# Kernel tuning notes

Hardware: AMD Instinct MI355X
Metric: run time of the kernel (lower is better)

The kernel has to match this reference:

```python
import jax, jax.numpy as jnp
import numpy as np

N, E = 32768, 262144
IN_C, OUT_C = 128, 128
N_GRAPHS = 64


def setup_inputs() -> dict:
    key = jax.random.key(0)
    ks = jax.random.split(key, 8)
    x = jax.random.normal(ks[0], (N, IN_C), dtype=jnp.float32)
    edge_index = jax.random.randint(ks[1], (2, E), 0, N, dtype=jnp.int32)
    batch = jnp.sort(jax.random.randint(ks[2], (N,), 0, N_GRAPHS, dtype=jnp.int32))
    rand = jax.random.uniform(ks[3], (E,), dtype=jnp.float32)  # replaces random.random() draws
    lim_t = 1.0 / np.sqrt(IN_C)
    W_t = jax.random.uniform(ks[4], (IN_C, OUT_C), jnp.float32, -lim_t, lim_t)
    b_t = jax.random.uniform(ks[5], (OUT_C,), jnp.float32, -lim_t, lim_t)
    lim_s = 1.0 / np.sqrt(OUT_C)
    W_s = jax.random.uniform(ks[6], (OUT_C, 1), jnp.float32, -lim_s, lim_s)
    b_s = jax.random.uniform(ks[7], (1,), jnp.float32, -lim_s, lim_s)
    return dict(x=x, edge_index=edge_index, batch=batch, rand=rand,
                W_t=W_t, b_t=b_t, W_s=W_s, b_s=b_s)


def _greedy_match(scores, src, dst, rand, n):
    """Sequential greedy edge matching over score-sorted edges.
    Returns (order, cid_sorted, n_merged): cid_sorted[i] is the cluster id
    assigned to sorted edge i, or -1 if rejected/skipped."""
    scores = jax.lax.stop_gradient(scores)  # indices are non-differentiable (torch uses .item())
    rand = jax.lax.stop_gradient(rand)
    order = jnp.argsort(-scores)
    s_o, d_o = src[order], dst[order]
    acc = rand[order] <= scores[order]  # torch: skip edge if r > edge_score

    def step(carry, inp):
        avail, nxt = carry
        s, t, a = inp
        ok = a & avail[s] & avail[t]
        cid = jnp.where(ok, nxt, -1)
        avail = avail.at[s].set(avail[s] & ~ok)
        avail = avail.at[t].set(avail[t] & ~ok)
        return (avail, nxt + ok.astype(jnp.int32)), cid

    (_, n_merged), cid_sorted = jax.lax.scan(
        step, (jnp.ones((n,), bool), jnp.int32(0)), (s_o, d_o, acc))
    return order, cid_sorted, n_merged


def reference(x, edge_index, batch, rand, W_t, b_t, W_s, b_s):
    n = x.shape[0]
    src, dst = edge_index[0], edge_index[1]
    # merge_edge_sum + transform (eval mode, dropout p=0)
    x_merged = (x[src] + x[dst]) @ W_t + b_t          # [E, OUT_C]
    x_self = (x + x) @ W_t + b_t                      # [N, OUT_C] (self-edge merge)
    e = jax.nn.sigmoid((x_merged @ W_s).reshape(-1) + b_s[0])  # [E] edge scores

    order, cid_sorted, n_merged = _greedy_match(e, src, dst, rand, n)
    ok = cid_sorted >= 0                              # accepted sorted edges
    s_o, d_o = src[order], dst[order]

    # node -> cluster assignment (sentinel index n is dropped)
    cluster = jnp.full((n,), -1, jnp.int32)
    cluster = cluster.at[jnp.where(ok, s_o, n)].set(cid_sorted, mode='drop')
    cluster = cluster.at[jnp.where(ok, d_o, n)].set(cid_sorted, mode='drop')
    remaining = cluster < 0
    rem_rank = jnp.cumsum(remaining.astype(jnp.int32)) - 1  # ascending node order, like set iteration
    cluster = jnp.where(remaining, n_merged + rem_rank, cluster)
    num_clusters = n_merged + remaining.sum().astype(jnp.int32)

    # pooled features, padded to [n, OUT_C]; rows [0, num_clusters) are valid
    mcid = jnp.where(ok, cid_sorted, n)
    new_x = jnp.zeros((n, x_merged.shape[1]), x.dtype)
    new_x = new_x.at[mcid].set(x_merged[order], mode='drop')
    new_x = new_x.at[jnp.where(remaining, cluster, n)].set(x_self, mode='drop')

    # per-cluster edge score (1.0 for unmerged singleton nodes)
    new_edge_score = jnp.ones((n,), e.dtype).at[mcid].set(e[order], mode='drop')

    # new batch vector: new_batch[cluster[v]] = batch[v]
    new_batch = jnp.zeros((n,), batch.dtype).at[cluster].set(batch)

    # remapped edges + coalesce/remove_self_loops expressed as a validity mask
    new_ei = cluster[edge_index]                      # [2, E]
    key = new_ei[0].astype(jnp.int64) * n + new_ei[1].astype(jnp.int64)
    perm = jnp.argsort(key)
    ksorted = key[perm]
    first = jnp.concatenate([jnp.array([True]), ksorted[1:] != ksorted[:-1]])
    unique = jnp.zeros((key.shape[0],), bool).at[perm].set(first)
    edge_valid = unique & (new_ei[0] != new_ei[1])

    return new_x, cluster, new_batch, new_edge_score, num_clusters, new_ei, edge_valid, e
```

## Files before the change

kernel.cpp:

```cpp
#include <hip/hip_runtime.h>
#include <stdint.h>

typedef unsigned int u32;
typedef unsigned long long u64;

#define NN 32768
#define NE 262144
#define NC 128

#define O0 0u
#define O1 4194304u
#define O2 4227072u
#define O3 4259840u
#define O4 4292608u
#define O5 4292609u
#define O6 4816897u
#define O7 5079041u

#define HCAP (1u<<19)
#define NFULL 8
#define CNT0 8
#define MCAP 16384
#define SCAP 32768
#define SNB 32
#define MAXK 0xFFFFFFFFFFFFFFFFull
#define EMASK 0x3FFFFu

__global__ void ep_init(const float* Wt, const float* Ws, const float* bt, const float* bs,
                        double* u, double* c0, u32* counters,
                        u64* b0, u64* b1, u32* avail, int* cl,
                        u32* tkey, u32* tmin, unsigned char* premat) {
    u32 i = blockIdx.x*blockDim.x + threadIdx.x;
    if (blockIdx.x == 0 && threadIdx.x < 128) {
        int r = threadIdx.x;
        double s = 0.0;
        for (int j = 0; j < NC; j++) s += (double)Wt[r*NC+j] * (double)Ws[j];
        u[r] = s;
        if (r == 0) {
            double c = 0.0;
            for (int j = 0; j < NC; j++) c += (double)bt[j] * (double)Ws[j];
            *c0 = c + (double)bs[0];
        }
    }
    if (i < 64) counters[i] = 0u;
    if (i < NN) { b0[i] = MAXK; b1[i] = MAXK; cl[i] = -1; }
    if (i < NN/32) avail[i] = 0xFFFFFFFFu;
    ((unsigned short*)premat)[i] = 0;
    for (u32 j = i; j < HCAP; j += 131072u) { tkey[j] = 0xFFFFFFFFu; tmin[j] = 0xFFFFFFFFu; }
}

__global__ void ep_ynode(const float* x, const double* u, double* y) {
    int gid = blockIdx.x*blockDim.x + threadIdx.x;
    int v = gid >> 6, lane = threadIdx.x & 63;
    if (v >= NN) return;
    double t = (double)x[v*NC+lane]*u[lane] + (double)x[v*NC+lane+64]*u[lane+64];
    for (int off = 32; off; off >>= 1) t += __shfl_down(t, off, 64);
    if (lane == 0) y[v] = t;
}

__global__ void ep_escore(const int* src, const int* dst, const float* rnd, const double* y,
                          const double* c0, u64* fkey, u32* counters, float* out) {
    int e = blockIdx.x*blockDim.x + threadIdx.x;
    if (e >= NE) return;
    int s = src[e], d = dst[e];
    double z = y[s] + y[d] + *c0;
    double sc = 1.0/(1.0 + exp(-z));
    out[O7 + e] = (float)sc;
    u64 b = (u64)__double_as_longlong(z);
    u64 ord = (b & 0x8000000000000000ull) ? ~b : (b | 0x8000000000000000ull);
    u64 P = ((~ord) & 0xFFFFFFFFFFFC0000ull) | (u64)(u32)e;
    if ((double)rnd[e] <= sc) {
        u32 p = atomicAdd(&counters[CNT0], 1u);
        fkey[p] = P;
    }
}

__device__ __forceinline__ bool ep_bit(const u32* a, u32 v) { return (a[v>>5] >> (v&31)) & 1u; }

__global__ void ep_rA(const u64* fkey, const int* src, const int* dst,
                      const u32* cnt, u64* bt, const u32* avail) {
    u32 n = *cnt;
    for (u32 i = blockIdx.x*blockDim.x + threadIdx.x; i < n; i += 65536u) {
        u64 P = fkey[i];
        u32 e = (u32)(P & EMASK);
        u32 s = (u32)src[e], d = (u32)dst[e];
        if (ep_bit(avail, s) && ep_bit(avail, d)) {
            atomicMin(&bt[s], P); atomicMin(&bt[d], P);
        }
    }
}

__global__ void ep_rB(const u64* fkey, const int* src, const int* dst,
                      const u32* cnt, u32* cntN, u64* fkeyN,
                      const u64* bt, u64* btN, u32* avail,
                      u64* mkey, unsigned char* premat, u32* counters) {
    u32 n = *cnt;
    for (u32 i = blockIdx.x*blockDim.x + threadIdx.x; i < n; i += 65536u) {
        u64 P = fkey[i];
        u32 e = (u32)(P & EMASK);
        u32 s = (u32)src[e], d = (u32)dst[e];
        if (!ep_bit(avail, s) || !ep_bit(avail, d)) continue;
        if (bt[s] == P && bt[d] == P) {
            u32 slot = atomicAdd(&counters[2], 1u);
            mkey[slot] = P;
            premat[e] = 1;
            atomicAnd(&avail[s>>5], ~(1u<<(s&31)));
            atomicAnd(&avail[d>>5], ~(1u<<(d&31)));
        } else {
            u32 p = atomicAdd(cntN, 1u);
            fkeyN[p] = P;
            btN[s] = MAXK; btN[d] = MAXK;
        }
    }
}

__global__ void ep_merge(const u64* mk, const u64* fk, u32* counters, u64* ck) {
    u32 i = blockIdx.x*blockDim.x + threadIdx.x;
    u32 nm0 = counters[2];
    u32 cr  = counters[CNT0+NFULL];
    if (i == 0) { u32 tot = nm0 + cr; counters[4] = tot > SCAP ? SCAP : tot; }
    u64 K = MAXK;
    if (i < nm0) K = mk[i];
    else if (i < nm0 + cr && i < SCAP) K = fk[i-nm0];
    ck[i] = K;
}

__device__ __forceinline__ u64 ep_peers(u32 d, bool real) {
    u64 m = ~0ull;
    #pragma unroll
    for (int b = 0; b < 8; b++) {
        u64 bb = __ballot((d >> b) & 1u);
        m &= ((d >> b) & 1u) ? bb : ~bb;
    }
    return m & __ballot(real);
}

__global__ void ms_hist(const u64* key, u32* hist, int shift, const u32* counters) {
    __shared__ u32 h[256];
    int t = threadIdx.x;
    u32 total = counters[4];
    h[t] = 0; h[t+64] = 0; h[t+128] = 0; h[t+192] = 0;
    u32 blk = blockIdx.x;
    for (int j = 0; j < 16; j++) {
        u32 idx = blk*1024u + (u32)j*64u + (u32)t;
        bool real = idx < total;
        u64 k = real ? key[idx] : MAXK;
        u32 d = (u32)(k >> shift) & 255u;
        u64 m = ep_peers(d, real);
        if (real && t == (__ffsll((unsigned long long)m) - 1)) h[d] += (u32)__popcll(m);
    }
    hist[(u32)t*SNB + blk]       = h[t];
    hist[((u32)t+64)*SNB + blk]  = h[t+64];
    hist[((u32)t+128)*SNB + blk] = h[t+128];
    hist[((u32)t+192)*SNB + blk] = h[t+192];
}

__global__ void ms_scan(u32* hist) {
    __shared__ u32 w[4];
    int t = threadIdx.x;
    int base = t*32;
    u32 s = 0;
    for (int j = 0; j < 32; j++) s += hist[base+j];
    u32 x = s;
    for (int off = 1; off < 64; off <<= 1) { u32 yv = __shfl_up(x, off, 64); if ((t&63) >= off) x += yv; }
    if ((t&63) == 63) w[t>>6] = x;
    __syncthreads();
    if (t == 0) { u32 a = 0; for (int k = 0; k < 4; k++) { u32 tmp = w[k]; w[k] = a; a += tmp; } }
    __syncthreads();
    u32 run = w[t>>6] + x - s;
    for (int j = 0; j < 32; j++) { u32 tmp = hist[base+j]; hist[base+j] = run; run += tmp; }
}

__global__ void ms_scat(const u64* ki, u64* ko, const u32* hist, int shift, const u32* counters) {
    __shared__ u32 cnt[256];
    int t = threadIdx.x;
    u32 total = counters[4];
    cnt[t] = 0; cnt[t+64] = 0; cnt[t+128] = 0; cnt[t+192] = 0;
    u32 blk = blockIdx.x;
    for (int j = 0; j < 16; j++) {
        u32 idx = blk*1024u + (u32)j*64u + (u32)t;
        bool real = idx < total;
        u64 k = real ? ki[idx] : MAXK;
        u32 d = (u32)(k >> shift) & 255u;
        u64 m = ep_peers(d, real);
        if (real) {
            u32 rank = (u32)__popcll(m & (((u64)1 << t) - 1ull));
            int leader = __ffsll((unsigned long long)m) - 1;
            u32 base = 0;
            if (t == leader) { base = cnt[d]; cnt[d] = base + (u32)__popcll(m); }
            base = __shfl(base, leader, 64);
            ko[hist[d*SNB + blk] + base + rank] = k;
        }
    }
}

__global__ void ep_csum(const u64* sk, const unsigned char* premat, const u32* counters,
                        u32* mflag, u32* csums) {
    u32 i = blockIdx.x*1024 + threadIdx.x;
    u32 cnt = counters[4];
    bool pre = (i < cnt) && premat[(u32)(sk[i] & EMASK)];
    bool cand = (i < cnt) && !pre;
    mflag[i] = pre ? 1u : 0u;
    int c = __syncthreads_count(cand ? 1 : 0);
    if (threadIdx.x == 0) csums[blockIdx.x] = (u32)c;
}

__global__ void ep_cscan(u32* csums, u32* counters, int which) {
    int t = threadIdx.x;
    u32 v = (t < SNB) ? csums[t] : 0u;
    u32 x = v;
    for (int off = 1; off < 64; off <<= 1) { u32 y = __shfl_up(x, off, 64); if (t >= off) x += y; }
    if (t < SNB) csums[t] = x - v;
    if (t == SNB-1) counters[which] = x;
}

__global__ void ep_cemit(const u64* sk, const unsigned char* premat, const u32* counters,
                         const u32* csums, u32* candIdx) {
    __shared__ u32 w[16];
    int t = threadIdx.x;
    u32 i = blockIdx.x*1024 + t;
    u32 cnt = counters[4];
    bool pre = (i < cnt) && premat[(u32)(sk[i] & EMASK)];
    u32 c = ((i < cnt) && !pre) ? 1u : 0u;
    u32 x = c;
    for (int off = 1; off < 64; off <<= 1) { u32 y = __shfl_up(x, off, 64); if ((t&63) >= off) x += y; }
    if ((t&63) == 63) w[t>>6] = x;
    __syncthreads();
    if (t < 16) {
        u32 ww = w[t];
        for (int off = 1; off < 16; off <<= 1) { u32 y = __shfl_up(ww, off, 16); if (t >= off) ww += y; }
        w[t] = ww;
    }
    __syncthreads();
    u32 excl = ((t>>6) ? w[(t>>6)-1] : 0u) + x - c;
    if (c) candIdx[csums[blockIdx.x] + excl] = i;
}

__global__ void __launch_bounds__(512) ep_walk(const u64* sk, const int* src, const int* dst,
                                               const u32* candIdx, u32* counters,
                                               const u32* availG, u32* mflag, u32* msums) {
    __shared__ u32 avail[1024];
    __shared__ u32 claim[16384];
    __shared__ u32 part[512];
    __shared__ u32 segs[32];
    int t = threadIdx.x;
    avail[t] = availG[t]; avail[t+512] = availG[t+512];
    for (int j = t; j < 16384; j += 512) claim[j] = 0xFFFFFFFFu;
    __syncthreads();
    u32 ncand = counters[5];
    u32 iterTag = 0x3FFFFFu;
    for (u32 base = 0; base < ncand; base += 512) {
        u32 j = base + (u32)t;
        bool have = j < ncand;
        u32 i = 0, s = 0, d = 0;
        if (have) {
            i = candIdx[j];
            u32 e = (u32)(sk[i] & EMASK);
            s = (u32)src[e]; d = (u32)dst[e];
        }
        u32 hs = s & 16383u, hd = d & 16383u;
        int st = 1;
        if (have && ((avail[s>>5]>>(s&31))&1u) && ((avail[d>>5]>>(d&31))&1u)) st = 0;
        for (int guard = 0; guard < 4096; guard++) {
            u32 tag = (iterTag << 10) | (u32)t;
            if (st == 0) { atomicMin(&claim[hs], tag); atomicMin(&claim[hd], tag); }
            __syncthreads();
            if (st == 0) {
                bool aok = ((avail[s>>5]>>(s&31))&1u) && ((avail[d>>5]>>(d&31))&1u);
                if (!aok) st = 1;
                else if (claim[hs] == tag && claim[hd] == tag) {
                    st = 2;
                    atomicAnd(&avail[s>>5], ~(1u<<(s&31)));
                    atomicAnd(&avail[d>>5], ~(1u<<(d&31)));
                    mflag[i] = 1u;
                }
            }
            iterTag--;
            if (__syncthreads_count(st == 0) == 0) break;
        }
    }
    __syncthreads();
    u32 p = 0; int b2 = t*64;
    for (int j = 0; j < 64; j++) p += mflag[b2+j];
    part[t] = p;
    __syncthreads();
    if (t < 32) { u32 sg = 0; for (int j = 0; j < 16; j++) sg += part[t*16+j]; segs[t] = sg; }
    __syncthreads();
    if (t == 0) { u32 a = 0; for (int g = 0; g < 32; g++) { msums[g] = a; a += segs[g]; } counters[2] = a; }
}

__global__ void ep_memit(const u64* sk, const int* src, const int* dst,
                         const u32* mflag, const u32* msums,
                         const int* batch, u64* Mlist, int* cl, float* out) {
    __shared__ u32 w[16];
    int t = threadIdx.x;
    u32 i = blockIdx.x*1024 + t;
    u32 m = mflag[i];
    u32 x = m;
    for (int off = 1; off < 64; off <<= 1) { u32 y = __shfl_up(x, off, 64); if ((t&63) >= off) x += y; }
    if ((t&63) == 63) w[t>>6] = x;
    __syncthreads();
    if (t < 16) {
        u32 ww = w[t];
        for (int off = 1; off < 16; off <<= 1) { u32 y = __shfl_up(ww, off, 16); if (t >= off) ww += y; }
        w[t] = ww;
    }
    __syncthreads();
    u32 excl = ((t>>6) ? w[(t>>6)-1] : 0u) + x - m;
    if (m) {
        u32 cid = msums[blockIdx.x] + excl;
        u32 e = (u32)(sk[i] & EMASK);
        u32 s = (u32)src[e], d = (u32)dst[e];
        Mlist[cid] = ((u64)e << 30) | ((u64)s << 15) | (u64)d;
        cl[s] = (int)cid; cl[d] = (int)cid;
        u32 mx = s > d ? s : d;
        out[O2 + cid] = (float)batch[mx];
        out[O3 + cid] = out[O7 + e];
    }
}

__global__ void ep_scanN(int* cl, u32* counters, u32* slist, float* out) {
    __shared__ u32 w[16];
    int t = threadIdx.x;
    int base = t*32;
    u32 s = 0;
    for (int j = 0; j < 32; j++) s += (cl[base+j] < 0) ? 1u : 0u;
    u32 x = s;
    for (int off = 1; off < 64; off <<= 1) { u32 y = __shfl_up(x, off, 64); if ((t&63) >= off) x += y; }
    if ((t&63) == 63) w[t>>6] = x;
    __syncthreads();
    if (t < 16) {
        u32 ww = w[t];
        for (int off = 1; off < 16; off <<= 1) { u32 y = __shfl_up(ww, off, 16); if (t >= off) ww += y; }
        w[t] = ww;
    }
    __syncthreads();
    u32 excl = ((t>>6) ? w[(t>>6)-1] : 0u) + x - s;
    u32 total = w[15];
    u32 nm = counters[2];
    if (t == 0) {
        counters[3] = nm + total;
        counters[6] = total;
        out[O4] = (float)(nm + total);
    }
    u32 run = nm + excl;
    for (int j = 0; j < 32; j++) {
        if (cl[base+j] < 0) {
            slist[run - nm] = (u32)(base + j);
            cl[base+j] = (int)(run++);
        }
    }
}

__global__ void ep_out_nodes(const int* cl, const int* batch, const u32* counters, float* out) {
    int v = blockIdx.x*blockDim.x + threadIdx.x;
    if (v >= NN) return;
    u32 nm = counters[2], ncl = counters[3];
    int c = cl[v];
    out[O1 + v] = (float)c;
    if (c >= (int)nm) out[O2 + c] = (float)batch[v];
    if (v >= (int)nm) out[O3 + v] = 1.0f;
    if (v >= (int)ncl) out[O2 + v] = 0.0f;
}

__global__ void ep_newx_m(const float* x, const float* Wt, const float* bt,
                          const u64* Mlist, const u32* counters, float* out) {
    __shared__ u64 ml[32];
    __shared__ float m[32][128];
    u32 nm = counters[2];
    u32 base = blockIdx.x * 32u;
    if (base >= nm) return;
    int t = threadIdx.x, lane = t & 63, wv = t >> 6;
    if (t < 32) { u32 r = base + (u32)t; ml[t] = (r < nm) ? Mlist[r] : 0ull; }
    __syncthreads();
    for (int i = t; i < 4096; i += 256) {
        int r = i >> 7, k = i & 127;
        u64 v = ml[r];
        u32 s = (u32)((v>>15)&0x7FFF), d = (u32)(v&0x7FFF);
        m[r][k] = x[s*NC+k] + x[d*NC+k];
    }
    __syncthreads();
    float a0[8], a1[8];
    #pragma unroll
    for (int r = 0; r < 8; r++) { a0[r] = bt[lane]; a1[r] = bt[lane+64]; }
    for (int k = 0; k < 128; k++) {
        float w0 = Wt[k*NC+lane], w1 = Wt[k*NC+lane+64];
        #pragma unroll
        for (int r = 0; r < 8; r++) { float mm = m[wv*8+r][k]; a0[r] += mm*w0; a1[r] += mm*w1; }
    }
    #pragma unroll
    for (int r = 0; r < 8; r++) {
        u32 row = base + (u32)(wv*8 + r);
        if (row < nm) {
            out[O0 + (size_t)row*NC + lane]      = a0[r];
            out[O0 + (size_t)row*NC + lane + 64] = a1[r];
        }
    }
}

__global__ void ep_newx_s(const float* x, const float* Wt, const float* bt,
                          const u32* slist, const u32* counters, float* out) {
    __shared__ u32 nodes[32];
    __shared__ float m[32][128];
    u32 nm = counters[2], ncl = counters[3], sc = counters[6];
    u32 base = nm + blockIdx.x * 32u;
    if (base >= NN) return;
    int t = threadIdx.x, lane = t & 63, wv = t >> 6;
    if (base >= ncl) {
        for (int i = t; i < 4096; i += 256) {
            u32 row = base + (u32)(i >> 7);
            if (row < NN) out[O0 + (size_t)row*NC + (i & 127)] = 0.0f;
        }
        return;
    }
    if (t < 32) { u32 p = base - nm + (u32)t; nodes[t] = (p < sc) ? slist[p] : slist[0]; }
    __syncthreads();
    for (int i = t; i < 4096; i += 256) {
        int r = i >> 7, k = i & 127;
        m[r][k] = 2.0f * x[nodes[r]*NC + k];
    }
    __syncthreads();
    float a0[8], a1[8];
    #pragma unroll
    for (int r = 0; r < 8; r++) { a0[r] = bt[lane]; a1[r] = bt[lane+64]; }
    for (int k = 0; k < 128; k++) {
        float w0 = Wt[k*NC+lane], w1 = Wt[k*NC+lane+64];
        #pragma unroll
        for (int r = 0; r < 8; r++) { float mm = m[wv*8+r][k]; a0[r] += mm*w0; a1[r] += mm*w1; }
    }
    #pragma unroll
    for (int r = 0; r < 8; r++) {
        u32 row = base + (u32)(wv*8 + r);
        if (row >= NN) continue;
        if (row < ncl) {
            out[O0 + (size_t)row*NC + lane]      = a0[r];
            out[O0 + (size_t)row*NC + lane + 64] = a1[r];
        } else {
            out[O0 + (size_t)row*NC + lane]      = 0.0f;
            out[O0 + (size_t)row*NC + lane + 64] = 0.0f;
        }
    }
}

__global__ void ep_newei(const int* src, const int* dst, const int* cl,
                         u32* tkey, u32* tmin, u32* eslot, float* out) {
    int e = blockIdx.x*blockDim.x + threadIdx.x;
    if (e >= NE) return;
    u32 cs = (u32)cl[src[e]], cd = (u32)cl[dst[e]];
    out[O5 + e]      = (float)cs;
    out[O5 + NE + e] = (float)cd;
    u32 key = (cs << 15) | cd;
    u32 slot = ((key * 2654435761u) >> 11) & (HCAP-1);
    while (true) {
        u32 k = tkey[slot];
        if (k == key) break;
        if (k == 0xFFFFFFFFu) {
            u32 old = atomicCAS(&tkey[slot], 0xFFFFFFFFu, key);
            if (old == 0xFFFFFFFFu || old == key) break;
        }
        slot = (slot + 1) & (HCAP-1);
    }
    eslot[e] = slot | ((cs != cd) ? 0x80000000u : 0u);
    atomicMin(&tmin[slot], (u32)e);
}

__global__ void ep_valid(const u32* tmin, const u32* eslot, float* out) {
    int e = blockIdx.x*blockDim.x + threadIdx.x;
    if (e >= NE) return;
    u32 sl = eslot[e];
    bool valid = (tmin[sl & 0x7FFFFFFFu] == (u32)e) && (sl >> 31);
    out[O6 + e] = valid ? 1.0f : 0.0f;
}

extern "C" void kernel_launch(void* const* d_in, const int* in_sizes, int n_in,
                              void* d_out, int out_size, void* d_ws, size_t ws_size,
                              hipStream_t stream) {
    (void)in_sizes; (void)n_in; (void)out_size; (void)ws_size;
    const float* x    = (const float*)d_in[0];
    const int*   ei   = (const int*)d_in[1];
    const int*   src  = ei;
    const int*   dst  = ei + NE;
    const int*   batch= (const int*)d_in[2];
    const float* rnd  = (const float*)d_in[3];
    const float* Wt   = (const float*)d_in[4];
    const float* bt   = (const float*)d_in[5];
    const float* Ws   = (const float*)d_in[6];
    const float* bs   = (const float*)d_in[7];
    float* out = (float*)d_out;

    char* w = (char*)d_ws;
    double* u  = (double*)w;
    double* c0 = (double*)(w + 1024);
    u32* counters = (u32*)(w + 2048);
    size_t off = 4096;
    double* y   = (double*)(w + off); off += (size_t)NN*8;
    u64* fkeyA  = (u64*)(w + off); off += (size_t)NE*8;
    u64* fkeyB  = (u64*)(w + off); off += (size_t)NE*8;
    u64* mkeyA  = (u64*)(w + off); off += (size_t)MCAP*8;
    u64* combK  = (u64*)(w + off); off += (size_t)SCAP*8;
    u64* combK2 = (u64*)(w + off); off += (size_t)SCAP*8;
    u64* bt0    = (u64*)(w + off); off += (size_t)NN*8;
    u64* bt1    = (u64*)(w + off); off += (size_t)NN*8;
    u32* avail  = (u32*)(w + off); off += NN/8;
    int* cl     = (int*)(w + off); off += (size_t)NN*4;
    u64* Mlist  = (u64*)(w + off); off += (size_t)NN*8;
    u32* hist   = (u32*)(w + off); off += 8192*4;
    u32* mflag  = (u32*)(w + off); off += (size_t)SCAP*4;
    u32* candIdx= (u32*)(w + off); off += (size_t)SCAP*4;
    u32* csums  = (u32*)(w + off); off += 64*4;
    u32* msums  = (u32*)(w + off); off += 64*4;
    u32* slist  = (u32*)(w + off); off += (size_t)NN*4;
    unsigned char* premat = (unsigned char*)(w + off); off += NE;
    u32* tkey   = (u32*)(w + off); off += (size_t)HCAP*4;
    u32* tmin   = (u32*)(w + off); off += (size_t)HCAP*4;
    u32* eslot  = (u32*)(w + off); off += (size_t)NE*4;

    ep_init<<<512, 256, 0, stream>>>(Wt, Ws, bt, bs, u, c0, counters,
                                     bt0, bt1, avail, cl, tkey, tmin, premat);
    ep_ynode<<<8192, 256, 0, stream>>>(x, u, y);
    ep_escore<<<1024, 256, 0, stream>>>(src, dst, rnd, y, c0, fkeyA, counters, out);

    u64 *fk = fkeyA, *fk2 = fkeyB;
    u64 *bc = bt0, *bn = bt1;
    for (u32 rd = 0; rd < NFULL; rd++) {
        ep_rA<<<256, 256, 0, stream>>>(fk, src, dst, &counters[CNT0+rd], bc, avail);
        ep_rB<<<256, 256, 0, stream>>>(fk, src, dst, &counters[CNT0+rd], &counters[CNT0+rd+1],
                                       fk2, bc, bn, avail, mkeyA, premat, counters);
        u64* tp;
        tp = fk; fk = fk2; fk2 = tp;
        tp = bc; bc = bn; bn = tp;
    }

    ep_merge<<<SNB, 1024, 0, stream>>>(mkeyA, fk, counters, combK);
    u64 *ki = combK, *ko = combK2;
    for (int p = 0; p < 6; p++) {
        int shift = 16 + p*8;
        ms_hist<<<SNB, 64, 0, stream>>>(ki, hist, shift, counters);
        ms_scan<<<1, 256, 0, stream>>>(hist);
        ms_scat<<<SNB, 64, 0, stream>>>(ki, ko, hist, shift, counters);
        u64* tp = ki; ki = ko; ko = tp;
    }

    ep_csum<<<SNB, 1024, 0, stream>>>(combK, premat, counters, mflag, csums);
    ep_cscan<<<1, 64, 0, stream>>>(csums, counters, 5);
    ep_cemit<<<SNB, 1024, 0, stream>>>(combK, premat, counters, csums, candIdx);
    ep_walk<<<1, 512, 0, stream>>>(combK, src, dst, candIdx, counters, avail, mflag, msums);
    ep_memit<<<SNB, 1024, 0, stream>>>(combK, src, dst, mflag, msums, batch, Mlist, cl, out);

    ep_scanN<<<1, 1024, 0, stream>>>(cl, counters, slist, out);
    ep_out_nodes<<<128, 256, 0, stream>>>(cl, batch, counters, out);

    ep_newx_m<<<512, 256, 0, stream>>>(x, Wt, bt, Mlist, counters, out);
    ep_newx_s<<<1024, 256, 0, stream>>>(x, Wt, bt, slist, counters, out);

    ep_newei<<<1024, 256, 0, stream>>>(src, dst, cl, tkey, tmin, eslot, out);
    ep_valid<<<1024, 256, 0, stream>>>(tmin, eslot, out);
}
```

Before: 717.4 us.

## Fuse radix sort passes into one persistent kernel and merge walk stages

The six-pass radix sort, previously three launches per pass, becomes a single persistent 32-block kernel that separates hist, scan and scatter with a software grid barrier built on global atomics. The candidate compaction, greedy walk, merged-list emission and singleton scan, previously six separate kernels, are folded into one 1024-thread single-block kernel. The aim is to cut roughly two dozen small kernel launches and their serialization gaps. In exchange it relies on all 32 blocks being co-resident for the spin barrier, and it moves the emit and scan work onto a single block.

```diff
diff --git a/kernel.cpp b/kernel.cpp
--- a/kernel.cpp
+++ b/kernel.cpp
@@ -135,121 +135,123 @@
     return m & __ballot(real);
 }
 
-__global__ void ms_hist(const u64* key, u32* hist, int shift, const u32* counters) {
+__device__ __forceinline__ void ms_gbar(u32* bar) {
+    __syncthreads();
+    if (threadIdx.x == 0) {
+        __threadfence();
+        u32 gen = atomicAdd(&bar[1], 0u);
+        if (atomicAdd(&bar[0], 1u) == SNB - 1) {
+            atomicExch(&bar[0], 0u);
+            __threadfence();
+            atomicAdd(&bar[1], 1u);
+        } else {
+            while (atomicAdd(&bar[1], 0u) == gen) __builtin_amdgcn_s_sleep(8);
+        }
+        __threadfence();
+    }
+    __syncthreads();
+}
+
+__global__ void __launch_bounds__(64) ms_sort(u64* a, u64* b, u32* hist,
+                                              const u32* counters, u32* bar) {
     __shared__ u32 h[256];
     int t = threadIdx.x;
+    u32 blk = blockIdx.x;
     u32 total = counters[4];
-    h[t] = 0; h[t+64] = 0; h[t+128] = 0; h[t+192] = 0;
-    u32 blk = blockIdx.x;
-    for (int j = 0; j < 16; j++) {
-        u32 idx = blk*1024u + (u32)j*64u + (u32)t;
-        bool real = idx < total;
-        u64 k = real ? key[idx] : MAXK;
-        u32 d = (u32)(k >> shift) & 255u;
-        u64 m = ep_peers(d, real);
-        if (real && t == (__ffsll((unsigned long long)m) - 1)) h[d] += (u32)__popcll(m);
-    }
-    hist[(u32)t*SNB + blk]       = h[t];
-    hist[((u32)t+64)*SNB + blk]  = h[t+64];
-    hist[((u32)t+128)*SNB + blk] = h[t+128];
-    hist[((u32)t+192)*SNB + blk] = h[t+192];
-}
-
-__global__ void ms_scan(u32* hist) {
-    __shared__ u32 w[4];
-    int t = threadIdx.x;
-    int base = t*32;
-    u32 s = 0;
-    for (int j = 0; j < 32; j++) s += hist[base+j];
-    u32 x = s;
-    for (int off = 1; off < 64; off <<= 1) { u32 yv = __shfl_up(x, off, 64); if ((t&63) >= off) x += yv; }
-    if ((t&63) == 63) w[t>>6] = x;
-    __syncthreads();
-    if (t == 0) { u32 a = 0; for (int k = 0; k < 4; k++) { u32 tmp = w[k]; w[k] = a; a += tmp; } }
-    __syncthreads();
-    u32 run = w[t>>6] + x - s;
-    for (int j = 0; j < 32; j++) { u32 tmp = hist[base+j]; hist[base+j] = run; run += tmp; }
-}
-
-__global__ void ms_scat(const u64* ki, u64* ko, const u32* hist, int shift, const u32* counters) {
-    __shared__ u32 cnt[256];
-    int t = threadIdx.x;
-    u32 total = counters[4];
-    cnt[t] = 0; cnt[t+64] = 0; cnt[t+128] = 0; cnt[t+192] = 0;
-    u32 blk = blockIdx.x;
-    for (int j = 0; j < 16; j++) {
-        u32 idx = blk*1024u + (u32)j*64u + (u32)t;
-        bool real = idx < total;
-        u64 k = real ? ki[idx] : MAXK;
-        u32 d = (u32)(k >> shift) & 255u;
-        u64 m = ep_peers(d, real);
-        if (real) {
-            u32 rank = (u32)__popcll(m & (((u64)1 << t) - 1ull));
-            int leader = __ffsll((unsigned long long)m) - 1;
-            u32 base = 0;
-            if (t == leader) { base = cnt[d]; cnt[d] = base + (u32)__popcll(m); }
-            base = __shfl(base, leader, 64);
-            ko[hist[d*SNB + blk] + base + rank] = k;
-        }
-    }
-}
-
-__global__ void ep_csum(const u64* sk, const unsigned char* premat, const u32* counters,
-                        u32* mflag, u32* csums) {
-    u32 i = blockIdx.x*1024 + threadIdx.x;
-    u32 cnt = counters[4];
-    bool pre = (i < cnt) && premat[(u32)(sk[i] & EMASK)];
-    bool cand = (i < cnt) && !pre;
-    mflag[i] = pre ? 1u : 0u;
-    int c = __syncthreads_count(cand ? 1 : 0);
-    if (threadIdx.x == 0) csums[blockIdx.x] = (u32)c;
-}
-
-__global__ void ep_cscan(u32* csums, u32* counters, int which) {
-    int t = threadIdx.x;
-    u32 v = (t < SNB) ? csums[t] : 0u;
-    u32 x = v;
-    for (int off = 1; off < 64; off <<= 1) { u32 y = __shfl_up(x, off, 64); if (t >= off) x += y; }
-    if (t < SNB) csums[t] = x - v;
-    if (t == SNB-1) counters[which] = x;
-}
-
-__global__ void ep_cemit(const u64* sk, const unsigned char* premat, const u32* counters,
-                         const u32* csums, u32* candIdx) {
-    __shared__ u32 w[16];
-    int t = threadIdx.x;
-    u32 i = blockIdx.x*1024 + t;
-    u32 cnt = counters[4];
-    bool pre = (i < cnt) && premat[(u32)(sk[i] & EMASK)];
-    u32 c = ((i < cnt) && !pre) ? 1u : 0u;
-    u32 x = c;
-    for (int off = 1; off < 64; off <<= 1) { u32 y = __shfl_up(x, off, 64); if ((t&63) >= off) x += y; }
-    if ((t&63) == 63) w[t>>6] = x;
-    __syncthreads();
-    if (t < 16) {
-        u32 ww = w[t];
-        for (int off = 1; off < 16; off <<= 1) { u32 y = __shfl_up(ww, off, 16); if (t >= off) ww += y; }
-        w[t] = ww;
-    }
-    __syncthreads();
-    u32 excl = ((t>>6) ? w[(t>>6)-1] : 0u) + x - c;
-    if (c) candIdx[csums[blockIdx.x] + excl] = i;
-}
-
-__global__ void __launch_bounds__(512) ep_walk(const u64* sk, const int* src, const int* dst,
-                                               const u32* candIdx, u32* counters,
-                                               const u32* availG, u32* mflag, u32* msums) {
+    u64 *ki = a, *ko = b;
+    for (int p = 0; p < 6; p++) {
+        int shift = 16 + p*8;
+        h[t] = 0; h[t+64] = 0; h[t+128] = 0; h[t+192] = 0;
+        for (int j = 0; j < 16; j++) {
+            u32 idx = blk*1024u + (u32)j*64u + (u32)t;
+            bool real = idx < total;
+            u64 k = real ? ki[idx] : MAXK;
+            u32 d = (u32)(k >> shift) & 255u;
+            u64 m = ep_peers(d, real);
+            if (real && t == (__ffsll((unsigned long long)m) - 1)) h[d] += (u32)__popcll(m);
+        }
+        hist[(u32)t*SNB + blk]       = h[t];
+        hist[((u32)t+64)*SNB + blk]  = h[t+64];
+        hist[((u32)t+128)*SNB + blk] = h[t+128];
+        hist[((u32)t+192)*SNB + blk] = h[t+192];
+        ms_gbar(bar);
+        if (blk == 0) {
+            int b2 = t*128;
+            u32 s = 0;
+            for (int j = 0; j < 128; j++) s += hist[b2+j];
+            u32 x = s;
+            for (int off = 1; off < 64; off <<= 1) { u32 yv = __shfl_up(x, off, 64); if (t >= off) x += yv; }
+            u32 run = x - s;
+            for (int j = 0; j < 128; j++) { u32 tmp = hist[b2+j]; hist[b2+j] = run; run += tmp; }
+        }
+        ms_gbar(bar);
+        h[t] = 0; h[t+64] = 0; h[t+128] = 0; h[t+192] = 0;
+        for (int j = 0; j < 16; j++) {
+            u32 idx = blk*1024u + (u32)j*64u + (u32)t;
+            bool real = idx < total;
+            u64 k = real ? ki[idx] : MAXK;
+            u32 d = (u32)(k >> shift) & 255u;
+            u64 m = ep_peers(d, real);
+            if (real) {
+                u32 rank = (u32)__popcll(m & (((u64)1 << t) - 1ull));
+                int leader = __ffsll((unsigned long long)m) - 1;
+                u32 base = 0;
+                if (t == leader) { base = h[d]; h[d] = base + (u32)__popcll(m); }
+                base = __shfl(base, leader, 64);
+                ko[hist[d*SNB + blk] + base + rank] = k;
+            }
+        }
+        ms_gbar(bar);
+        u64* tp = ki; ki = ko; ko = tp;
+    }
+}
+
+__global__ void __launch_bounds__(1024) ep_walk(const u64* sk, const int* src, const int* dst,
+                                                const unsigned char* premat, u32* counters,
+                                                const u32* availG, u32* mflag, u32* candIdx,
+                                                u64* Mlist, int* cl, u32* slist,
+                                                const int* batch, float* out) {
     __shared__ u32 avail[1024];
     __shared__ u32 claim[16384];
-    __shared__ u32 part[512];
-    __shared__ u32 segs[32];
+    __shared__ u32 wsc[16];
     int t = threadIdx.x;
-    avail[t] = availG[t]; avail[t+512] = availG[t+512];
-    for (int j = t; j < 16384; j += 512) claim[j] = 0xFFFFFFFFu;
-    __syncthreads();
-    u32 ncand = counters[5];
+    avail[t] = availG[t];
+    for (int j = t; j < 16384; j += 1024) claim[j] = 0xFFFFFFFFu;
+    u32 total = counters[4];
+    int b32 = t*32;
+
+    u32 premask = 0, havemask = 0, cc = 0;
+    for (int j = 0; j < 32; j++) {
+        u32 i = (u32)(b32 + j);
+        u32 have = (i < total) ? 1u : 0u;
+        u32 pre = 0;
+        if (have) pre = premat[(u32)(sk[i] & EMASK)] ? 1u : 0u;
+        mflag[i] = pre;
+        premask |= pre << j;
+        havemask |= have << j;
+        cc += have & ~pre & 1u;
+    }
+    __syncthreads();
+    u32 x = cc;
+    for (int off = 1; off < 64; off <<= 1) { u32 y = __shfl_up(x, off, 64); if ((t&63) >= off) x += y; }
+    if ((t&63) == 63) wsc[t>>6] = x;
+    __syncthreads();
+    if (t < 16) {
+        u32 ww = wsc[t];
+        for (int off = 1; off < 16; off <<= 1) { u32 y = __shfl_up(ww, off, 16); if (t >= off) ww += y; }
+        wsc[t] = ww;
+    }
+    __syncthreads();
+    u32 cbase = ((t>>6) ? wsc[(t>>6)-1] : 0u) + x - cc;
+    u32 ncand = wsc[15];
+    for (int j = 0; j < 32; j++) {
+        if (((havemask>>j)&1u) && !((premask>>j)&1u)) candIdx[cbase++] = (u32)(b32+j);
+    }
+    __threadfence_block();
+    __syncthreads();
+
     u32 iterTag = 0x3FFFFFu;
-    for (u32 base = 0; base < ncand; base += 512) {
+    for (u32 base = 0; base < ncand; base += 1024) {
         u32 j = base + (u32)t;
         bool have = j < ncand;
         u32 i = 0, s = 0, d = 0;
@@ -279,75 +281,70 @@
             if (__syncthreads_count(st == 0) == 0) break;
         }
     }
-    __syncthreads();
-    u32 p = 0; int b2 = t*64;
-    for (int j = 0; j < 64; j++) p += mflag[b2+j];
-    part[t] = p;
-    __syncthreads();
-    if (t < 32) { u32 sg = 0; for (int j = 0; j < 16; j++) sg += part[t*16+j]; segs[t] = sg; }
-    __syncthreads();
-    if (t == 0) { u32 a = 0; for (int g = 0; g < 32; g++) { msums[g] = a; a += segs[g]; } counters[2] = a; }
-}
-
-__global__ void ep_memit(const u64* sk, const int* src, const int* dst,
-                         const u32* mflag, const u32* msums,
-                         const int* batch, u64* Mlist, int* cl, float* out) {
-    __shared__ u32 w[16];
-    int t = threadIdx.x;
-    u32 i = blockIdx.x*1024 + t;
-    u32 m = mflag[i];
-    u32 x = m;
+    __threadfence_block();
+    __syncthreads();
+
+    u32 mc = 0, mmask = 0;
+    for (int j = 0; j < 32; j++) {
+        u32 f = mflag[b32+j] & 1u;
+        mmask |= f << j;
+        mc += f;
+    }
+    __syncthreads();
+    x = mc;
     for (int off = 1; off < 64; off <<= 1) { u32 y = __shfl_up(x, off, 64); if ((t&63) >= off) x += y; }
-    if ((t&63) == 63) w[t>>6] = x;
+    if ((t&63) == 63) wsc[t>>6] = x;
     __syncthreads();
     if (t < 16) {
-        u32 ww = w[t];
+        u32 ww = wsc[t];
         for (int off = 1; off < 16; off <<= 1) { u32 y = __shfl_up(ww, off, 16); if (t >= off) ww += y; }
-        w[t] = ww;
-    }
-    __syncthreads();
-    u32 excl = ((t>>6) ? w[(t>>6)-1] : 0u) + x - m;
-    if (m) {
-        u32 cid = msums[blockIdx.x] + excl;
-        u32 e = (u32)(sk[i] & EMASK);
-        u32 s = (u32)src[e], d = (u32)dst[e];
-        Mlist[cid] = ((u64)e << 30) | ((u64)s << 15) | (u64)d;
-        cl[s] = (int)cid; cl[d] = (int)cid;
-        u32 mx = s > d ? s : d;
-        out[O2 + cid] = (float)batch[mx];
-        out[O3 + cid] = out[O7 + e];
-    }
-}
-
-__global__ void ep_scanN(int* cl, u32* counters, u32* slist, float* out) {
-    __shared__ u32 w[16];
-    int t = threadIdx.x;
-    int base = t*32;
-    u32 s = 0;
-    for (int j = 0; j < 32; j++) s += (cl[base+j] < 0) ? 1u : 0u;
-    u32 x = s;
+        wsc[t] = ww;
+    }
+    __syncthreads();
+    u32 mbase = ((t>>6) ? wsc[(t>>6)-1] : 0u) + x - mc;
+    u32 nm = wsc[15];
+    if (t == 0) counters[2] = nm;
+    for (int j = 0; j < 32; j++) {
+        if ((mmask>>j)&1u) {
+            u32 i = (u32)(b32+j);
+            u32 e = (u32)(sk[i] & EMASK);
+            u32 s = (u32)src[e], d = (u32)dst[e];
+            Mlist[mbase] = ((u64)e << 30) | ((u64)s << 15) | (u64)d;
+            cl[s] = (int)mbase; cl[d] = (int)mbase;
+            u32 mx = s > d ? s : d;
+            out[O2 + mbase] = (float)batch[mx];
+            out[O3 + mbase] = out[O7 + e];
+            mbase++;
+        }
+    }
+    __threadfence_block();
+    __syncthreads();
+
+    u32 sc2 = 0;
+    for (int j = 0; j < 32; j++) sc2 += (cl[b32+j] < 0) ? 1u : 0u;
+    __syncthreads();
+    x = sc2;
     for (int off = 1; off < 64; off <<= 1) { u32 y = __shfl_up(x, off, 64); if ((t&63) >= off) x += y; }
-    if ((t&63) == 63) w[t>>6] = x;
+    if ((t&63) == 63) wsc[t>>6] = x;
     __syncthreads();
     if (t < 16) {
-        u32 ww = w[t];
+        u32 ww = wsc[t];
         for (int off = 1; off < 16; off <<= 1) { u32 y = __shfl_up(ww, off, 16); if (t >= off) ww += y; }
-        w[t] = ww;
-    }
-    __syncthreads();
-    u32 excl = ((t>>6) ? w[(t>>6)-1] : 0u) + x - s;
-    u32 total = w[15];
-    u32 nm = counters[2];
+        wsc[t] = ww;
+    }
+    __syncthreads();
+    u32 excl = ((t>>6) ? wsc[(t>>6)-1] : 0u) + x - sc2;
+    u32 stotal = wsc[15];
     if (t == 0) {
-        counters[3] = nm + total;
-        counters[6] = total;
-        out[O4] = (float)(nm + total);
+        counters[3] = nm + stotal;
+        counters[6] = stotal;
+        out[O4] = (float)(nm + stotal);
     }
     u32 run = nm + excl;
     for (int j = 0; j < 32; j++) {
-        if (cl[base+j] < 0) {
-            slist[run - nm] = (u32)(base + j);
-            cl[base+j] = (int)(run++);
+        if (cl[b32+j] < 0) {
+            slist[run - nm] = (u32)(b32 + j);
+            cl[b32+j] = (int)(run++);
         }
     }
 }
@@ -507,8 +504,6 @@
     u32* hist   = (u32*)(w + off); off += 8192*4;
     u32* mflag  = (u32*)(w + off); off += (size_t)SCAP*4;
     u32* candIdx= (u32*)(w + off); off += (size_t)SCAP*4;
-    u32* csums  = (u32*)(w + off); off += 64*4;
-    u32* msums  = (u32*)(w + off); off += 64*4;
     u32* slist  = (u32*)(w + off); off += (size_t)NN*4;
     unsigned char* premat = (unsigned char*)(w + off); off += NE;
     u32* tkey   = (u32*)(w + off); off += (size_t)HCAP*4;
@@ -532,22 +527,11 @@
     }
 
     ep_merge<<<SNB, 1024, 0, stream>>>(mkeyA, fk, counters, combK);
-    u64 *ki = combK, *ko = combK2;
-    for (int p = 0; p < 6; p++) {
-        int shift = 16 + p*8;
-        ms_hist<<<SNB, 64, 0, stream>>>(ki, hist, shift, counters);
-        ms_scan<<<1, 256, 0, stream>>>(hist);
-        ms_scat<<<SNB, 64, 0, stream>>>(ki, ko, hist, shift, counters);
-        u64* tp = ki; ki = ko; ko = tp;
-    }
-
-    ep_csum<<<SNB, 1024, 0, stream>>>(combK, premat, counters, mflag, csums);
-    ep_cscan<<<1, 64, 0, stream>>>(csums, counters, 5);
-    ep_cemit<<<SNB, 1024, 0, stream>>>(combK, premat, counters, csums, candIdx);
-    ep_walk<<<1, 512, 0, stream>>>(combK, src, dst, candIdx, counters, avail, mflag, msums);
-    ep_memit<<<SNB, 1024, 0, stream>>>(combK, src, dst, mflag, msums, batch, Mlist, cl, out);
-
-    ep_scanN<<<1, 1024, 0, stream>>>(cl, counters, slist, out);
+    ms_sort<<<SNB, 64, 0, stream>>>(combK, combK2, hist, counters, &counters[32]);
+
+    ep_walk<<<1, 1024, 0, stream>>>(combK, src, dst, premat, counters, avail,
+                                    mflag, candIdx, Mlist, cl, slist, batch, out);
+
     ep_out_nodes<<<128, 256, 0, stream>>>(cl, batch, counters, out);
 
     ep_newx_m<<<512, 256, 0, stream>>>(x, Wt, bt, Mlist, counters, out);
```

After: 940.2 us. 31.0% more time.

## Fuse radix sort passes into one persistent kernel and fold candidate compaction into walk

Applied to the files above, without the earlier changes.

Replaces the 18 per-pass radix sort launches (hist/scan/scatter over 6 digits) with a single persistent 32-block kernel that uses a software grid barrier built on global atomics between phases. It also removes the candidate-compaction kernels (csum/cscan/cemit) and lets the single-block walk kernel, widened to 1024 threads, scan all sorted entries directly, marking pre-matched entries itself. The goal is to cut kernel launch overhead and small serial kernels. In exchange the walk now visits pre-matched entries as well, the grid barrier depends on all 32 blocks being co-resident, and mflag is now zeroed in init.

```diff
diff --git a/kernel.cpp b/kernel.cpp
--- a/kernel.cpp
+++ b/kernel.cpp
@@ -29,7 +29,7 @@
 __global__ void ep_init(const float* Wt, const float* Ws, const float* bt, const float* bs,
                         double* u, double* c0, u32* counters,
                         u64* b0, u64* b1, u32* avail, int* cl,
-                        u32* tkey, u32* tmin, unsigned char* premat) {
+                        u32* tkey, u32* tmin, unsigned char* premat, u32* mflag) {
     u32 i = blockIdx.x*blockDim.x + threadIdx.x;
     if (blockIdx.x == 0 && threadIdx.x < 128) {
         int r = threadIdx.x;
@@ -45,6 +45,7 @@
     if (i < 64) counters[i] = 0u;
     if (i < NN) { b0[i] = MAXK; b1[i] = MAXK; cl[i] = -1; }
     if (i < NN/32) avail[i] = 0xFFFFFFFFu;
+    if (i < SCAP) mflag[i] = 0u;
     ((unsigned short*)premat)[i] = 0;
     for (u32 j = i; j < HCAP; j += 131072u) { tkey[j] = 0xFFFFFFFFu; tmin[j] = 0xFFFFFFFFu; }
 }
@@ -135,132 +136,105 @@
     return m & __ballot(real);
 }
 
-__global__ void ms_hist(const u64* key, u32* hist, int shift, const u32* counters) {
+__device__ __forceinline__ void ms_gbar(u32* bar) {
+    __syncthreads();
+    if (threadIdx.x == 0) {
+        __threadfence();
+        u32 gen = atomicAdd(&bar[1], 0u);
+        if (atomicAdd(&bar[0], 1u) == SNB - 1) {
+            atomicExch(&bar[0], 0u);
+            __threadfence();
+            atomicAdd(&bar[1], 1u);
+        } else {
+            while (atomicAdd(&bar[1], 0u) == gen) __builtin_amdgcn_s_sleep(8);
+        }
+        __threadfence();
+    }
+    __syncthreads();
+}
+
+__global__ void __launch_bounds__(64) ms_sort(u64* a, u64* b, u32* hist,
+                                              const u32* counters, u32* bar) {
     __shared__ u32 h[256];
     int t = threadIdx.x;
+    u32 blk = blockIdx.x;
     u32 total = counters[4];
-    h[t] = 0; h[t+64] = 0; h[t+128] = 0; h[t+192] = 0;
-    u32 blk = blockIdx.x;
-    for (int j = 0; j < 16; j++) {
-        u32 idx = blk*1024u + (u32)j*64u + (u32)t;
-        bool real = idx < total;
-        u64 k = real ? key[idx] : MAXK;
-        u32 d = (u32)(k >> shift) & 255u;
-        u64 m = ep_peers(d, real);
-        if (real && t == (__ffsll((unsigned long long)m) - 1)) h[d] += (u32)__popcll(m);
-    }
-    hist[(u32)t*SNB + blk]       = h[t];
-    hist[((u32)t+64)*SNB + blk]  = h[t+64];
-    hist[((u32)t+128)*SNB + blk] = h[t+128];
-    hist[((u32)t+192)*SNB + blk] = h[t+192];
-}
-
-__global__ void ms_scan(u32* hist) {
-    __shared__ u32 w[4];
-    int t = threadIdx.x;
-    int base = t*32;
-    u32 s = 0;
-    for (int j = 0; j < 32; j++) s += hist[base+j];
-    u32 x = s;
-    for (int off = 1; off < 64; off <<= 1) { u32 yv = __shfl_up(x, off, 64); if ((t&63) >= off) x += yv; }
-    if ((t&63) == 63) w[t>>6] = x;
-    __syncthreads();
-    if (t == 0) { u32 a = 0; for (int k = 0; k < 4; k++) { u32 tmp = w[k]; w[k] = a; a += tmp; } }
-    __syncthreads();
-    u32 run = w[t>>6] + x - s;
-    for (int j = 0; j < 32; j++) { u32 tmp = hist[base+j]; hist[base+j] = run; run += tmp; }
-}
-
-__global__ void ms_scat(const u64* ki, u64* ko, const u32* hist, int shift, const u32* counters) {
-    __shared__ u32 cnt[256];
-    int t = threadIdx.x;
-    u32 total = counters[4];
-    cnt[t] = 0; cnt[t+64] = 0; cnt[t+128] = 0; cnt[t+192] = 0;
-    u32 blk = blockIdx.x;
-    for (int j = 0; j < 16; j++) {
-        u32 idx = blk*1024u + (u32)j*64u + (u32)t;
-        bool real = idx < total;
-        u64 k = real ? ki[idx] : MAXK;
-        u32 d = (u32)(k >> shift) & 255u;
-        u64 m = ep_peers(d, real);
-        if (real) {
-            u32 rank = (u32)__popcll(m & (((u64)1 << t) - 1ull));
-            int leader = __ffsll((unsigned long long)m) - 1;
-            u32 base = 0;
-            if (t == leader) { base = cnt[d]; cnt[d] = base + (u32)__popcll(m); }
-            base = __shfl(base, leader, 64);
-            ko[hist[d*SNB + blk] + base + rank] = k;
-        }
-    }
-}
-
-__global__ void ep_csum(const u64* sk, const unsigned char* premat, const u32* counters,
-                        u32* mflag, u32* csums) {
-    u32 i = blockIdx.x*1024 + threadIdx.x;
-    u32 cnt = counters[4];
-    bool pre = (i < cnt) && premat[(u32)(sk[i] & EMASK)];
-    bool cand = (i < cnt) && !pre;
-    mflag[i] = pre ? 1u : 0u;
-    int c = __syncthreads_count(cand ? 1 : 0);
-    if (threadIdx.x == 0) csums[blockIdx.x] = (u32)c;
-}
-
-__global__ void ep_cscan(u32* csums, u32* counters, int which) {
-    int t = threadIdx.x;
-    u32 v = (t < SNB) ? csums[t] : 0u;
-    u32 x = v;
-    for (int off = 1; off < 64; off <<= 1) { u32 y = __shfl_up(x, off, 64); if (t >= off) x += y; }
-    if (t < SNB) csums[t] = x - v;
-    if (t == SNB-1) counters[which] = x;
-}
-
-__global__ void ep_cemit(const u64* sk, const unsigned char* premat, const u32* counters,
-                         const u32* csums, u32* candIdx) {
-    __shared__ u32 w[16];
-    int t = threadIdx.x;
-    u32 i = blockIdx.x*1024 + t;
-    u32 cnt = counters[4];
-    bool pre = (i < cnt) && premat[(u32)(sk[i] & EMASK)];
-    u32 c = ((i < cnt) && !pre) ? 1u : 0u;
-    u32 x = c;
-    for (int off = 1; off < 64; off <<= 1) { u32 y = __shfl_up(x, off, 64); if ((t&63) >= off) x += y; }
-    if ((t&63) == 63) w[t>>6] = x;
-    __syncthreads();
-    if (t < 16) {
-        u32 ww = w[t];
-        for (int off = 1; off < 16; off <<= 1) { u32 y = __shfl_up(ww, off, 16); if (t >= off) ww += y; }
-        w[t] = ww;
-    }
-    __syncthreads();
-    u32 excl = ((t>>6) ? w[(t>>6)-1] : 0u) + x - c;
-    if (c) candIdx[csums[blockIdx.x] + excl] = i;
-}
-
-__global__ void __launch_bounds__(512) ep_walk(const u64* sk, const int* src, const int* dst,
-                                               const u32* candIdx, u32* counters,
-                                               const u32* availG, u32* mflag, u32* msums) {
+    u64 *ki = a, *ko = b;
+    for (int p = 0; p < 6; p++) {
+        int shift = 16 + p*8;
+        h[t] = 0; h[t+64] = 0; h[t+128] = 0; h[t+192] = 0;
+        for (int j = 0; j < 16; j++) {
+            u32 idx = blk*1024u + (u32)j*64u + (u32)t;
+            bool real = idx < total;
+            u64 k = real ? ki[idx] : MAXK;
+            u32 d = (u32)(k >> shift) & 255u;
+            u64 m = ep_peers(d, real);
+            if (real && t == (__ffsll((unsigned long long)m) - 1)) h[d] += (u32)__popcll(m);
+        }
+        hist[(u32)t*SNB + blk]       = h[t];
+        hist[((u32)t+64)*SNB + blk]  = h[t+64];
+        hist[((u32)t+128)*SNB + blk] = h[t+128];
+        hist[((u32)t+192)*SNB + blk] = h[t+192];
+        ms_gbar(bar);
+        if (blk == 0) {
+            int b2 = t*128;
+            u32 s = 0;
+            for (int j = 0; j < 128; j++) s += hist[b2+j];
+            u32 x = s;
+            for (int off = 1; off < 64; off <<= 1) { u32 yv = __shfl_up(x, off, 64); if (t >= off) x += yv; }
+            u32 run = x - s;
+            for (int j = 0; j < 128; j++) { u32 tmp = hist[b2+j]; hist[b2+j] = run; run += tmp; }
+        }
+        ms_gbar(bar);
+        h[t] = 0; h[t+64] = 0; h[t+128] = 0; h[t+192] = 0;
+        for (int j = 0; j < 16; j++) {
+            u32 idx = blk*1024u + (u32)j*64u + (u32)t;
+            bool real = idx < total;
+            u64 k = real ? ki[idx] : MAXK;
+            u32 d = (u32)(k >> shift) & 255u;
+            u64 m = ep_peers(d, real);
+            if (real) {
+                u32 rank = (u32)__popcll(m & (((u64)1 << t) - 1ull));
+                int leader = __ffsll((unsigned long long)m) - 1;
+                u32 base = 0;
+                if (t == leader) { base = h[d]; h[d] = base + (u32)__popcll(m); }
+                base = __shfl(base, leader, 64);
+                ko[hist[d*SNB + blk] + base + rank] = k;
+            }
+        }
+        ms_gbar(bar);
+        u64* tp = ki; ki = ko; ko = tp;
+    }
+}
+
+__global__ void __launch_bounds__(1024) ep_walk(const u64* sk, const int* src, const int* dst,
+                                                const unsigned char* premat, u32* counters,
+                                                const u32* availG, u32* mflag, u32* msums) {
     __shared__ u32 avail[1024];
     __shared__ u32 claim[16384];
-    __shared__ u32 part[512];
+    __shared__ u32 part[1024];
     __shared__ u32 segs[32];
     int t = threadIdx.x;
-    avail[t] = availG[t]; avail[t+512] = availG[t+512];
-    for (int j = t; j < 16384; j += 512) claim[j] = 0xFFFFFFFFu;
-    __syncthreads();
-    u32 ncand = counters[5];
+    avail[t] = availG[t];
+    for (int j = t; j < 16384; j += 1024) claim[j] = 0xFFFFFFFFu;
+    __syncthreads();
+    u32 total = counters[4];
     u32 iterTag = 0x3FFFFFu;
-    for (u32 base = 0; base < ncand; base += 512) {
-        u32 j = base + (u32)t;
-        bool have = j < ncand;
-        u32 i = 0, s = 0, d = 0;
+    for (u32 base = 0; base < total; base += 1024) {
+        u32 i = base + (u32)t;
+        bool have = i < total;
+        u32 s = 0, d = 0;
+        int st = 1;
         if (have) {
-            i = candIdx[j];
             u32 e = (u32)(sk[i] & EMASK);
-            s = (u32)src[e]; d = (u32)dst[e];
+            if (premat[e]) {
+                mflag[i] = 1u;
+            } else {
+                s = (u32)src[e]; d = (u32)dst[e];
+                if (((avail[s>>5]>>(s&31))&1u) && ((avail[d>>5]>>(d&31))&1u)) st = 0;
+            }
         }
         u32 hs = s & 16383u, hd = d & 16383u;
-        int st = 1;
-        if (have && ((avail[s>>5]>>(s&31))&1u) && ((avail[d>>5]>>(d&31))&1u)) st = 0;
         for (int guard = 0; guard < 4096; guard++) {
             u32 tag = (iterTag << 10) | (u32)t;
             if (st == 0) { atomicMin(&claim[hs], tag); atomicMin(&claim[hd], tag); }
@@ -279,12 +253,13 @@
             if (__syncthreads_count(st == 0) == 0) break;
         }
     }
-    __syncthreads();
-    u32 p = 0; int b2 = t*64;
-    for (int j = 0; j < 64; j++) p += mflag[b2+j];
+    __threadfence_block();
+    __syncthreads();
+    u32 p = 0; int b2 = t*32;
+    for (int j = 0; j < 32; j++) p += mflag[b2+j];
     part[t] = p;
     __syncthreads();
-    if (t < 32) { u32 sg = 0; for (int j = 0; j < 16; j++) sg += part[t*16+j]; segs[t] = sg; }
+    if (t < 32) { u32 sg = 0; for (int j = 0; j < 32; j++) sg += part[t*32+j]; segs[t] = sg; }
     __syncthreads();
     if (t == 0) { u32 a = 0; for (int g = 0; g < 32; g++) { msums[g] = a; a += segs[g]; } counters[2] = a; }
 }
@@ -506,8 +481,6 @@
     u64* Mlist  = (u64*)(w + off); off += (size_t)NN*8;
     u32* hist   = (u32*)(w + off); off += 8192*4;
     u32* mflag  = (u32*)(w + off); off += (size_t)SCAP*4;
-    u32* candIdx= (u32*)(w + off); off += (size_t)SCAP*4;
-    u32* csums  = (u32*)(w + off); off += 64*4;
     u32* msums  = (u32*)(w + off); off += 64*4;
     u32* slist  = (u32*)(w + off); off += (size_t)NN*4;
     unsigned char* premat = (unsigned char*)(w + off); off += NE;
@@ -516,7 +489,7 @@
     u32* eslot  = (u32*)(w + off); off += (size_t)NE*4;
 
     ep_init<<<512, 256, 0, stream>>>(Wt, Ws, bt, bs, u, c0, counters,
-                                     bt0, bt1, avail, cl, tkey, tmin, premat);
+                                     bt0, bt1, avail, cl, tkey, tmin, premat, mflag);
     ep_ynode<<<8192, 256, 0, stream>>>(x, u, y);
     ep_escore<<<1024, 256, 0, stream>>>(src, dst, rnd, y, c0, fkeyA, counters, out);
 
@@ -532,19 +505,9 @@
     }
 
     ep_merge<<<SNB, 1024, 0, stream>>>(mkeyA, fk, counters, combK);
-    u64 *ki = combK, *ko = combK2;
-    for (int p = 0; p < 6; p++) {
-        int shift = 16 + p*8;
-        ms_hist<<<SNB, 64, 0, stream>>>(ki, hist, shift, counters);
-        ms_scan<<<1, 256, 0, stream>>>(hist);
-        ms_scat<<<SNB, 64, 0, stream>>>(ki, ko, hist, shift, counters);
-        u64* tp = ki; ki = ko; ko = tp;
-    }
-
-    ep_csum<<<SNB, 1024, 0, stream>>>(combK, premat, counters, mflag, csums);
-    ep_cscan<<<1, 64, 0, stream>>>(csums, counters, 5);
-    ep_cemit<<<SNB, 1024, 0, stream>>>(combK, premat, counters, csums, candIdx);
-    ep_walk<<<1, 512, 0, stream>>>(combK, src, dst, candIdx, counters, avail, mflag, msums);
+    ms_sort<<<SNB, 64, 0, stream>>>(combK, combK2, hist, counters, &counters[32]);
+
+    ep_walk<<<1, 1024, 0, stream>>>(combK, src, dst, premat, counters, avail, mflag, msums);
     ep_memit<<<SNB, 1024, 0, stream>>>(combK, src, dst, mflag, msums, batch, Mlist, cl, out);
 
     ep_scanN<<<1, 1024, 0, stream>>>(cl, counters, slist, out);
```

After: 772.9 us. +7.7%, slower.
